# Performance work log

Hardware: AMD Instinct MI355X
Metric: run time of the kernel (lower is better)

Reference implementation:

```python
import jax, jax.numpy as jnp
import numpy as np

N_NODES = 100000
N_EDGES = 1600000
N_PAIRS = 200000
IN_CH = 128
HID_CH = 128


def _graph_conv(x, src, dst, edge_weight, w_rel, b_rel, w_root, num_nodes):
    # PyG GraphConv with aggr='mean':
    # out = lin_rel(mean_{j in N(i)}(x_j * w_ij)) + lin_root(x_i)
    msg = x[src] * edge_weight[:, None]                       # [E, C] gather
    agg = jax.ops.segment_sum(msg, dst, num_segments=num_nodes)  # [N, C]
    cnt = jax.ops.segment_sum(jnp.ones((src.shape[0],), x.dtype), dst,
                              num_segments=num_nodes)          # in-degree
    agg = agg / jnp.maximum(cnt, 1.0)[:, None]                 # mean aggr
    return agg @ w_rel + b_rel + x @ w_root


def setup_inputs() -> dict:
    key = jax.random.key(0)
    ks = jax.random.split(key, 10)
    x = jax.random.normal(ks[0], (N_NODES, IN_CH), dtype=jnp.float32)
    edge_index = jax.random.randint(ks[1], (2, N_EDGES), 0, N_NODES, dtype=jnp.int32)
    edge_weight = jax.random.uniform(ks[2], (N_EDGES,), dtype=jnp.float32)
    edge_label_index = jax.random.randint(ks[3], (2, N_PAIRS), 0, N_NODES, dtype=jnp.int32)
    s1 = 1.0 / np.sqrt(IN_CH)
    s2 = 1.0 / np.sqrt(HID_CH)
    w1_rel = jax.random.uniform(ks[4], (IN_CH, HID_CH), jnp.float32, -s1, s1)
    b1_rel = jnp.zeros((HID_CH,), jnp.float32)
    w1_root = jax.random.uniform(ks[5], (IN_CH, HID_CH), jnp.float32, -s1, s1)
    w2_rel = jax.random.uniform(ks[6], (HID_CH, HID_CH), jnp.float32, -s2, s2)
    b2_rel = jnp.zeros((HID_CH,), jnp.float32)
    w2_root = jax.random.uniform(ks[7], (HID_CH, HID_CH), jnp.float32, -s2, s2)
    return {"x": x, "edge_index": edge_index, "edge_weight": edge_weight,
            "edge_label_index": edge_label_index,
            "w1_rel": w1_rel, "b1_rel": b1_rel, "w1_root": w1_root,
            "w2_rel": w2_rel, "b2_rel": b2_rel, "w2_root": w2_root}


def reference(x, edge_index, edge_weight, edge_label_index,
              w1_rel, b1_rel, w1_root, w2_rel, b2_rel, w2_root):
    src, dst = edge_index[0], edge_index[1]
    # encode
    h = _graph_conv(x, src, dst, edge_weight, w1_rel, b1_rel, w1_root, x.shape[0])
    h = jax.nn.relu(h)
    z = _graph_conv(h, src, dst, edge_weight, w2_rel, b2_rel, w2_root, x.shape[0])
    # decode: scaled dot product between candidate pair embeddings
    zs = z[edge_label_index[0]]   # [P, H]
    zd = z[edge_label_index[1]]   # [P, H]
    scale = z.shape[-1] ** 0.5
    return jnp.sum(zs * zd, axis=-1) / scale
```

## Files before the change

### kernel.cpp

```cpp
#include <hip/hip_runtime.h>

#define NN 100000
#define NE 1600000
#define NP 200000
#define CH 128
#define LK 264

#define BSH 6
#define NB  1563
#define G1  256
#define EPB (NE / G1)
#define CAP3 4096
#define NCAST 6250

typedef _Float16 f16x8 __attribute__((ext_vector_type(8)));
typedef _Float16 f16x4 __attribute__((ext_vector_type(4)));
typedef float f32x4 __attribute__((ext_vector_type(4)));

__global__ __launch_bounds__(256)
void fused_prep_kernel(const float* __restrict__ x, _Float16* __restrict__ xh,
                       const int* __restrict__ dst, int* __restrict__ hist,
                       const float* __restrict__ w1r, const float* __restrict__ w1o,
                       const float* __restrict__ w2r, const float* __restrict__ w2o,
                       _Float16* __restrict__ w1t, _Float16* __restrict__ w2t) {
    __shared__ int s_h[NB];
    const int bb = blockIdx.x, tid = threadIdx.x;
    if (bb < NCAST) {
        int i = bb * 256 + tid;
        const float4* p = (const float4*)x + (size_t)i * 2;
        float4 a = p[0], b = p[1];
        f16x8 o = { (_Float16)a.x, (_Float16)a.y, (_Float16)a.z, (_Float16)a.w,
                    (_Float16)b.x, (_Float16)b.y, (_Float16)b.z, (_Float16)b.w };
        *((f16x8*)xh + i) = o;
    } else if (bb < NCAST + G1) {
        int g = bb - NCAST;
        for (int i = tid; i < NB; i += 256) s_h[i] = 0;
        __syncthreads();
        int start = g * EPB, end = start + EPB;
        for (int e = start + tid; e < end; e += 256)
            atomicAdd(&s_h[dst[e] >> BSH], 1);
        __syncthreads();
        int* row = hist + (size_t)g * NB;
        for (int i = tid; i < NB; i += 256) row[i] = s_h[i];
    } else {
        int idx = (bb - NCAST - G1) * 256 + tid;
        int which = idx >> 15;
        int li = idx & 32767;
        int n = li >> 8, k = li & 255;
        const float* wr = which ? w2r : w1r;
        const float* wo = which ? w2o : w1o;
        _Float16* wt = which ? w2t : w1t;
        float v = (k < 128) ? wr[k * 128 + n] : wo[(k - 128) * 128 + n];
        wt[li] = (_Float16)v;
    }
}

__global__ __launch_bounds__(256)
void colscan_kernel(int* __restrict__ hist, int* __restrict__ totals) {
    int b = blockIdx.x * 4 + (threadIdx.x >> 6);
    if (b >= NB) return;
    int lane = threadIdx.x & 63;
    size_t base = (size_t)(lane * 4) * NB + b;
    int v0 = hist[base];
    int v1 = hist[base + NB];
    int v2 = hist[base + 2 * (size_t)NB];
    int v3 = hist[base + 3 * (size_t)NB];
    int s0 = v0, s1 = s0 + v1, s2 = s1 + v2, s3 = s2 + v3;
    int incl = s3;
#pragma unroll
    for (int off = 1; off < 64; off <<= 1) {
        int n = __shfl_up(incl, off, 64);
        if (lane >= off) incl += n;
    }
    int excl = incl - s3;
    hist[base] = excl;
    hist[base + NB] = excl + s0;
    hist[base + 2 * (size_t)NB] = excl + s1;
    hist[base + 3 * (size_t)NB] = excl + s2;
    if (lane == 63) totals[b] = incl;
}

__global__ __launch_bounds__(1024)
void scanB_kernel(const int* __restrict__ totals, int* __restrict__ base) {
    __shared__ int s[2048];
    int tid = threadIdx.x;
    for (int i = tid; i < 2048; i += 1024) s[i] = (i < NB) ? totals[i] : 0;
    __syncthreads();
    for (int off = 1; off < 2048; off <<= 1) {
        int i0 = tid, i1 = tid + 1024;
        int v0 = (i0 >= off) ? s[i0 - off] : 0;
        int v1 = (i1 >= off) ? s[i1 - off] : 0;
        __syncthreads();
        s[i0] += v0; s[i1] += v1;
        __syncthreads();
    }
    if (tid == 0) base[0] = 0;
    for (int i = tid; i < NB; i += 1024) base[i + 1] = s[i];
}

__global__ __launch_bounds__(512)
void bucket_scatter_kernel(const int* __restrict__ src, const int* __restrict__ dst,
                           const float* __restrict__ ew, const int* __restrict__ hist,
                           const int* __restrict__ base, int2* __restrict__ tmp) {
    __shared__ int s_cur[NB];
    const int* row = hist + (size_t)blockIdx.x * NB;
    for (int i = threadIdx.x; i < NB; i += 512) s_cur[i] = base[i] + row[i];
    __syncthreads();
    int start = blockIdx.x * EPB, end = start + EPB;
    for (int e = start + threadIdx.x; e < end; e += 512) {
        int d = dst[e];
        int b = d >> BSH;
        int pos = atomicAdd(&s_cur[b], 1);
        tmp[pos] = make_int2(src[e] | ((d & 63) << 17), __float_as_int(ew[e]));
    }
}

__global__ __launch_bounds__(512)
void bucket_finalize_kernel(const int2* __restrict__ tmp, const int* __restrict__ base,
                            int* __restrict__ row_ptr, int2* __restrict__ csr, int N) {
    __shared__ int2 s_e[CAP3];
    __shared__ int s_cnt[64], s_off[64];
    int b = blockIdx.x;
    int lo = base[b], hi = base[b + 1];
    int size = hi - lo;
    int nbase = b << BSH;
    int ncnt = min(64, N - nbase);
    int tid = threadIdx.x;
    if (tid < 64) s_cnt[tid] = 0;
    bool inlds = (size <= CAP3);
    __syncthreads();
    if (inlds) {
        for (int i = tid; i < size; i += 512) {
            int2 e = tmp[lo + i];
            s_e[i] = e;
            atomicAdd(&s_cnt[(e.x >> 17) & 63], 1);
        }
    } else {
        for (int i = tid; i < size; i += 512) {
            int2 e = tmp[lo + i];
            atomicAdd(&s_cnt[(e.x >> 17) & 63], 1);
        }
    }
    __syncthreads();
    if (tid == 0) {
        int run = 0;
        for (int i = 0; i < 64; i++) { int v = s_cnt[i]; s_off[i] = run; s_cnt[i] = run; run += v; }
    }
    __syncthreads();
    if (tid < ncnt) row_ptr[nbase + tid] = lo + s_off[tid];
    if (b == NB - 1 && tid == 0) row_ptr[N] = hi;
    if (inlds) {
        for (int i = tid; i < size; i += 512) {
            int2 e = s_e[i];
            int dl = (e.x >> 17) & 63;
            int p = atomicAdd(&s_cnt[dl], 1);
            csr[lo + p] = make_int2(e.x & 0x1FFFF, e.y);
        }
    } else {
        for (int i = tid; i < size; i += 512) {
            int2 e = tmp[lo + i];
            int dl = (e.x >> 17) & 63;
            int p = atomicAdd(&s_cnt[dl], 1);
            csr[lo + p] = make_int2(e.x & 0x1FFFF, e.y);
        }
    }
}

template <bool RELU>
__global__ __launch_bounds__(512)
void gatherlayer_kernel(const _Float16* __restrict__ feat, const int* __restrict__ row_ptr,
                        const int2* __restrict__ csr, const _Float16* __restrict__ wt,
                        const float* __restrict__ bias, _Float16* __restrict__ out, int N) {
    __shared__ _Float16 atile[64][LK];

    const int tid = threadIdx.x;
    const int nb = blockIdx.x << BSH;
    const int wave = tid >> 6;
    const int lane = tid & 63;
    const int q = lane >> 4;
    const int l16 = lane & 15;
    const int c8 = l16 << 3;

    for (int nn = 0; nn < 8; nn++) {
        int local_n = wave * 8 + nn;
        int node = nb + local_n;
        if (node >= N) break;
        int r0 = row_ptr[node], r1 = row_ptr[node + 1];
        float acc[8] = {0.f, 0.f, 0.f, 0.f, 0.f, 0.f, 0.f, 0.f};
        int r = r0 + q;
        if (r < r1) {
            int2 e = csr[r];
            f16x8 v = *(const f16x8*)&feat[(size_t)e.x * CH + c8];
            int2 e2; f16x8 v2;
            bool h2 = (r + 4) < r1;
            if (h2) { e2 = csr[r + 4]; v2 = *(const f16x8*)&feat[(size_t)e2.x * CH + c8]; }
            for (int r3 = r + 8; r3 < r1; r3 += 4) {
                int2 e3 = csr[r3];
                f16x8 v3 = *(const f16x8*)&feat[(size_t)e3.x * CH + c8];
                float w = __int_as_float(e.y);
#pragma unroll
                for (int j = 0; j < 8; j++) acc[j] += w * (float)v[j];
                e = e2; v = v2;
                e2 = e3; v2 = v3;
            }
            float w = __int_as_float(e.y);
#pragma unroll
            for (int j = 0; j < 8; j++) acc[j] += w * (float)v[j];
            if (h2) {
                float w2 = __int_as_float(e2.y);
#pragma unroll
                for (int j = 0; j < 8; j++) acc[j] += w2 * (float)v2[j];
            }
        }
#pragma unroll
        for (int j = 0; j < 8; j++) {
            acc[j] += __shfl_xor(acc[j], 16, 64);
            acc[j] += __shfl_xor(acc[j], 32, 64);
        }
        if (q == 0) {
            float inv = 1.0f / fmaxf((float)(r1 - r0), 1.0f);
            f16x8 o;
#pragma unroll
            for (int j = 0; j < 8; j++) o[j] = (_Float16)(acc[j] * inv);
            *(f16x8*)&atile[local_n][c8] = o;
        }
    }

    for (int i = tid; i < 64 * 16; i += 512) {
        int rrow = i >> 4;
        int cc8 = (i & 15) << 3;
        int gn = nb + rrow;
        f16x8 v = {};
        if (gn < N) v = *(const f16x8*)&feat[(size_t)gn * CH + cc8];
        *(f16x8*)&atile[rrow][128 + cc8] = v;
    }
    __syncthreads();

    f32x4 ac[4];
#pragma unroll
    for (int m = 0; m < 4; m++) ac[m] = (f32x4){0.f, 0.f, 0.f, 0.f};

    const int ncol = wave * 16 + l16;
    const int kq = q * 8;
#pragma unroll
    for (int ks = 0; ks < 8; ks++) {
        int kbase = ks * 32 + kq;
        f16x8 bf = *(const f16x8*)&wt[(size_t)ncol * 256 + kbase];
#pragma unroll
        for (int m = 0; m < 4; m++) {
            f16x8 af = *(const f16x8*)&atile[m * 16 + l16][kbase];
            ac[m] = __builtin_amdgcn_mfma_f32_16x16x32_f16(af, bf, ac[m], 0, 0, 0);
        }
    }

    float bv = bias[ncol];
#pragma unroll
    for (int m = 0; m < 4; m++) {
#pragma unroll
        for (int r = 0; r < 4; r++) {
            int node = nb + m * 16 + q * 4 + r;
            if (node >= N) continue;
            float v = ac[m][r] + bv;
            if (RELU) v = fmaxf(v, 0.f);
            out[(size_t)node * CH + ncol] = (_Float16)v;
        }
    }
}

__global__ void decode_kernel(const _Float16* __restrict__ z,
                              const int* __restrict__ ps,
                              const int* __restrict__ pd,
                              float* __restrict__ out, int P) {
    long tid = (long)blockIdx.x * blockDim.x + threadIdx.x;
    int p = (int)(tid >> 5);
    int lane = (int)(tid & 31);
    if (p >= P) return;
    int s = ps[p], d = pd[p];
    f16x4 a = *(const f16x4*)&z[(size_t)s * CH + lane * 4];
    f16x4 b = *(const f16x4*)&z[(size_t)d * CH + lane * 4];
    float v = (float)a[0] * (float)b[0] + (float)a[1] * (float)b[1]
            + (float)a[2] * (float)b[2] + (float)a[3] * (float)b[3];
#pragma unroll
    for (int off = 16; off > 0; off >>= 1) v += __shfl_xor(v, off, 64);
    if (lane == 0) out[p] = v * 0.08838834764831845f;
}

extern "C" void kernel_launch(void* const* d_in, const int* in_sizes, int n_in,
                              void* d_out, int out_size, void* d_ws, size_t ws_size,
                              hipStream_t stream) {
    const float* x       = (const float*)d_in[0];
    const int*   ei      = (const int*)d_in[1];
    const float* ew      = (const float*)d_in[2];
    const int*   eli     = (const int*)d_in[3];
    const float* w1_rel  = (const float*)d_in[4];
    const float* b1      = (const float*)d_in[5];
    const float* w1_root = (const float*)d_in[6];
    const float* w2_rel  = (const float*)d_in[7];
    const float* b2      = (const float*)d_in[8];
    const float* w2_root = (const float*)d_in[9];
    float* out = (float*)d_out;

    const int N = NN, E = NE, P = NP;
    const size_t hrow = (size_t)N * CH * sizeof(_Float16);

    char* ws = (char*)d_ws;
    size_t off = 0;
    auto alloc = [&](size_t bytes) { char* p = ws + off; off = (off + bytes + 15) & ~(size_t)15; return p; };
    _Float16* xh  = (_Float16*)alloc(hrow);
    _Float16* hh  = (_Float16*)alloc(hrow);
    _Float16* zh  = (_Float16*)alloc(hrow);
    int* hist     = (int*)alloc((size_t)G1 * NB * 4);
    int* totals   = (int*)alloc((size_t)NB * 4);
    int* base     = (int*)alloc((size_t)(NB + 1) * 4);
    int* row_ptr  = (int*)alloc((size_t)(N + 1) * 4);
    int2* tmp     = (int2*)alloc((size_t)E * 8);
    int2* csr     = (int2*)alloc((size_t)E * 8);
    _Float16* w1t = (_Float16*)alloc((size_t)128 * 256 * 2);
    _Float16* w2t = (_Float16*)alloc((size_t)128 * 256 * 2);

    const int* src = ei;
    const int* dst = ei + E;

    fused_prep_kernel<<<NCAST + G1 + 256, 256, 0, stream>>>(
        x, xh, dst, hist, w1_rel, w1_root, w2_rel, w2_root, w1t, w2t);

    colscan_kernel<<<(NB + 3) / 4, 256, 0, stream>>>(hist, totals);
    scanB_kernel<<<1, 1024, 0, stream>>>(totals, base);
    bucket_scatter_kernel<<<G1, 512, 0, stream>>>(src, dst, ew, hist, base, tmp);
    bucket_finalize_kernel<<<NB, 512, 0, stream>>>(tmp, base, row_ptr, csr, N);

    gatherlayer_kernel<true><<<NB, 512, 0, stream>>>(xh, row_ptr, csr, w1t, b1, hh, N);
    gatherlayer_kernel<false><<<NB, 512, 0, stream>>>(hh, row_ptr, csr, w2t, b2, zh, N);

    {
        long threads = (long)P * 32;
        decode_kernel<<<(int)((threads + 255) / 256), 256, 0, stream>>>(zh, eli, eli + P, out, P);
    }
}
```

Before: 365.7 us.

## Replace two-level bucket sort CSR build with per-node global atomic counting sort

Replaces the bucketed histogram, column scan and two-pass bucket scatter/finalize with a direct per-node in-degree count using global atomics, a two-kernel scan into row_ptr, and a single scatter into CSR via global atomic cursors. This drops the intermediate tmp buffer, one full pass over the edges and several launches. In exchange it relies on global atomics over 100k counters instead of LDS atomics. Edge order within each row becomes nondeterministic, so floating-point summation order can vary between runs.

```diff
diff --git a/kernel.cpp b/kernel.cpp
--- a/kernel.cpp
+++ b/kernel.cpp
@@ -10,8 +10,8 @@
 #define NB  1563
 #define G1  256
 #define EPB (NE / G1)
-#define CAP3 4096
 #define NCAST 6250
+#define NSB 196
 
 typedef _Float16 f16x8 __attribute__((ext_vector_type(8)));
 typedef _Float16 f16x4 __attribute__((ext_vector_type(4)));
@@ -19,11 +19,10 @@
 
 __global__ __launch_bounds__(256)
 void fused_prep_kernel(const float* __restrict__ x, _Float16* __restrict__ xh,
-                       const int* __restrict__ dst, int* __restrict__ hist,
+                       const int* __restrict__ dst, int* __restrict__ cnt,
                        const float* __restrict__ w1r, const float* __restrict__ w1o,
                        const float* __restrict__ w2r, const float* __restrict__ w2o,
                        _Float16* __restrict__ w1t, _Float16* __restrict__ w2t) {
-    __shared__ int s_h[NB];
     const int bb = blockIdx.x, tid = threadIdx.x;
     if (bb < NCAST) {
         int i = bb * 256 + tid;
@@ -34,14 +33,9 @@
         *((f16x8*)xh + i) = o;
     } else if (bb < NCAST + G1) {
         int g = bb - NCAST;
-        for (int i = tid; i < NB; i += 256) s_h[i] = 0;
-        __syncthreads();
         int start = g * EPB, end = start + EPB;
         for (int e = start + tid; e < end; e += 256)
-            atomicAdd(&s_h[dst[e] >> BSH], 1);
-        __syncthreads();
-        int* row = hist + (size_t)g * NB;
-        for (int i = tid; i < NB; i += 256) row[i] = s_h[i];
+            atomicAdd(&cnt[dst[e]], 1);
     } else {
         int idx = (bb - NCAST - G1) * 256 + tid;
         int which = idx >> 15;
@@ -55,114 +49,81 @@
     }
 }
 
-__global__ __launch_bounds__(256)
-void colscan_kernel(int* __restrict__ hist, int* __restrict__ totals) {
-    int b = blockIdx.x * 4 + (threadIdx.x >> 6);
-    if (b >= NB) return;
-    int lane = threadIdx.x & 63;
-    size_t base = (size_t)(lane * 4) * NB + b;
-    int v0 = hist[base];
-    int v1 = hist[base + NB];
-    int v2 = hist[base + 2 * (size_t)NB];
-    int v3 = hist[base + 3 * (size_t)NB];
-    int s0 = v0, s1 = s0 + v1, s2 = s1 + v2, s3 = s2 + v3;
-    int incl = s3;
+__global__ __launch_bounds__(512)
+void nodecount_sum_kernel(const int* __restrict__ cnt, int* __restrict__ bsum) {
+    __shared__ int s_w[8];
+    const int b = blockIdx.x, tid = threadIdx.x;
+    const int lane = tid & 63, w = tid >> 6;
+    int i = b * 512 + tid;
+    int v = (i < NN) ? cnt[i] : 0;
+#pragma unroll
+    for (int off = 1; off < 64; off <<= 1) v += __shfl_xor(v, off, 64);
+    if (lane == 0) s_w[w] = v;
+    __syncthreads();
+    if (tid == 0) {
+        int t = 0;
+#pragma unroll
+        for (int j = 0; j < 8; j++) t += s_w[j];
+        bsum[b] = t;
+    }
+}
+
+__global__ __launch_bounds__(512)
+void rowptr_kernel(const int* __restrict__ cnt, const int* __restrict__ bsum,
+                   int* __restrict__ row_ptr, int* __restrict__ cur) {
+    __shared__ int s_w[8];
+    __shared__ int s_woff[8];
+    __shared__ int s_boff;
+    const int b = blockIdx.x, tid = threadIdx.x;
+    const int lane = tid & 63, w = tid >> 6;
+
+    int v = (tid < b) ? bsum[tid] : 0;
+#pragma unroll
+    for (int off = 1; off < 64; off <<= 1) v += __shfl_xor(v, off, 64);
+    if (lane == 0) s_w[w] = v;
+    __syncthreads();
+    if (tid == 0) {
+        int t = 0;
+#pragma unroll
+        for (int j = 0; j < 8; j++) t += s_w[j];
+        s_boff = t;
+    }
+    __syncthreads();
+
+    int i = b * 512 + tid;
+    int c = (i < NN) ? cnt[i] : 0;
+    int incl = c;
 #pragma unroll
     for (int off = 1; off < 64; off <<= 1) {
         int n = __shfl_up(incl, off, 64);
         if (lane >= off) incl += n;
     }
-    int excl = incl - s3;
-    hist[base] = excl;
-    hist[base + NB] = excl + s0;
-    hist[base + 2 * (size_t)NB] = excl + s1;
-    hist[base + 3 * (size_t)NB] = excl + s2;
-    if (lane == 63) totals[b] = incl;
-}
-
-__global__ __launch_bounds__(1024)
-void scanB_kernel(const int* __restrict__ totals, int* __restrict__ base) {
-    __shared__ int s[2048];
-    int tid = threadIdx.x;
-    for (int i = tid; i < 2048; i += 1024) s[i] = (i < NB) ? totals[i] : 0;
-    __syncthreads();
-    for (int off = 1; off < 2048; off <<= 1) {
-        int i0 = tid, i1 = tid + 1024;
-        int v0 = (i0 >= off) ? s[i0 - off] : 0;
-        int v1 = (i1 >= off) ? s[i1 - off] : 0;
-        __syncthreads();
-        s[i0] += v0; s[i1] += v1;
-        __syncthreads();
-    }
-    if (tid == 0) base[0] = 0;
-    for (int i = tid; i < NB; i += 1024) base[i + 1] = s[i];
+    if (lane == 63) s_w[w] = incl;
+    __syncthreads();
+    if (tid == 0) {
+        int run = 0;
+#pragma unroll
+        for (int j = 0; j < 8; j++) { int t = s_w[j]; s_woff[j] = run; run += t; }
+    }
+    __syncthreads();
+    int excl = s_boff + s_woff[w] + incl - c;
+    if (i < NN) {
+        row_ptr[i] = excl;
+        cur[i] = excl;
+    }
+    if (b == NSB - 1 && tid == 511) row_ptr[NN] = s_boff + s_woff[7] + incl;
 }
 
 __global__ __launch_bounds__(512)
-void bucket_scatter_kernel(const int* __restrict__ src, const int* __restrict__ dst,
-                           const float* __restrict__ ew, const int* __restrict__ hist,
-                           const int* __restrict__ base, int2* __restrict__ tmp) {
-    __shared__ int s_cur[NB];
-    const int* row = hist + (size_t)blockIdx.x * NB;
-    for (int i = threadIdx.x; i < NB; i += 512) s_cur[i] = base[i] + row[i];
-    __syncthreads();
+void edge_scatter_kernel(const int* __restrict__ src, const int* __restrict__ dst,
+                         const float* __restrict__ ew, int* __restrict__ cur,
+                         int2* __restrict__ csr) {
     int start = blockIdx.x * EPB, end = start + EPB;
+#pragma unroll 4
     for (int e = start + threadIdx.x; e < end; e += 512) {
         int d = dst[e];
-        int b = d >> BSH;
-        int pos = atomicAdd(&s_cur[b], 1);
-        tmp[pos] = make_int2(src[e] | ((d & 63) << 17), __float_as_int(ew[e]));
-    }
-}
-
-__global__ __launch_bounds__(512)
-void bucket_finalize_kernel(const int2* __restrict__ tmp, const int* __restrict__ base,
-                            int* __restrict__ row_ptr, int2* __restrict__ csr, int N) {
-    __shared__ int2 s_e[CAP3];
-    __shared__ int s_cnt[64], s_off[64];
-    int b = blockIdx.x;
-    int lo = base[b], hi = base[b + 1];
-    int size = hi - lo;
-    int nbase = b << BSH;
-    int ncnt = min(64, N - nbase);
-    int tid = threadIdx.x;
-    if (tid < 64) s_cnt[tid] = 0;
-    bool inlds = (size <= CAP3);
-    __syncthreads();
-    if (inlds) {
-        for (int i = tid; i < size; i += 512) {
-            int2 e = tmp[lo + i];
-            s_e[i] = e;
-            atomicAdd(&s_cnt[(e.x >> 17) & 63], 1);
-        }
-    } else {
-        for (int i = tid; i < size; i += 512) {
-            int2 e = tmp[lo + i];
-            atomicAdd(&s_cnt[(e.x >> 17) & 63], 1);
-        }
-    }
-    __syncthreads();
-    if (tid == 0) {
-        int run = 0;
-        for (int i = 0; i < 64; i++) { int v = s_cnt[i]; s_off[i] = run; s_cnt[i] = run; run += v; }
-    }
-    __syncthreads();
-    if (tid < ncnt) row_ptr[nbase + tid] = lo + s_off[tid];
-    if (b == NB - 1 && tid == 0) row_ptr[N] = hi;
-    if (inlds) {
-        for (int i = tid; i < size; i += 512) {
-            int2 e = s_e[i];
-            int dl = (e.x >> 17) & 63;
-            int p = atomicAdd(&s_cnt[dl], 1);
-            csr[lo + p] = make_int2(e.x & 0x1FFFF, e.y);
-        }
-    } else {
-        for (int i = tid; i < size; i += 512) {
-            int2 e = tmp[lo + i];
-            int dl = (e.x >> 17) & 63;
-            int p = atomicAdd(&s_cnt[dl], 1);
-            csr[lo + p] = make_int2(e.x & 0x1FFFF, e.y);
-        }
+        int pos = atomicAdd(&cur[d], 1);
+        csr[pos] = make_int2(src[e], __float_as_int(ew[e]));
     }
 }
 
@@ -309,11 +270,10 @@
     _Float16* xh  = (_Float16*)alloc(hrow);
     _Float16* hh  = (_Float16*)alloc(hrow);
     _Float16* zh  = (_Float16*)alloc(hrow);
-    int* hist     = (int*)alloc((size_t)G1 * NB * 4);
-    int* totals   = (int*)alloc((size_t)NB * 4);
-    int* base     = (int*)alloc((size_t)(NB + 1) * 4);
+    int* cnt      = (int*)alloc((size_t)N * 4);
+    int* bsum     = (int*)alloc((size_t)NSB * 4);
     int* row_ptr  = (int*)alloc((size_t)(N + 1) * 4);
-    int2* tmp     = (int2*)alloc((size_t)E * 8);
+    int* cur      = (int*)alloc((size_t)N * 4);
     int2* csr     = (int2*)alloc((size_t)E * 8);
     _Float16* w1t = (_Float16*)alloc((size_t)128 * 256 * 2);
     _Float16* w2t = (_Float16*)alloc((size_t)128 * 256 * 2);
@@ -321,13 +281,14 @@
     const int* src = ei;
     const int* dst = ei + E;
 
+    hipMemsetAsync(cnt, 0, (size_t)N * 4, stream);
+
     fused_prep_kernel<<<NCAST + G1 + 256, 256, 0, stream>>>(
-        x, xh, dst, hist, w1_rel, w1_root, w2_rel, w2_root, w1t, w2t);
-
-    colscan_kernel<<<(NB + 3) / 4, 256, 0, stream>>>(hist, totals);
-    scanB_kernel<<<1, 1024, 0, stream>>>(totals, base);
-    bucket_scatter_kernel<<<G1, 512, 0, stream>>>(src, dst, ew, hist, base, tmp);
-    bucket_finalize_kernel<<<NB, 512, 0, stream>>>(tmp, base, row_ptr, csr, N);
+        x, xh, dst, cnt, w1_rel, w1_root, w2_rel, w2_root, w1t, w2t);
+
+    nodecount_sum_kernel<<<NSB, 512, 0, stream>>>(cnt, bsum);
+    rowptr_kernel<<<NSB, 512, 0, stream>>>(cnt, bsum, row_ptr, cur);
+    edge_scatter_kernel<<<G1, 512, 0, stream>>>(src, dst, ew, cur, csr);
 
     gatherlayer_kernel<true><<<NB, 512, 0, stream>>>(xh, row_ptr, csr, w1t, b1, hh, N);
     gatherlayer_kernel<false><<<NB, 512, 0, stream>>>(hh, row_ptr, csr, w2t, b2, zh, N);
```

Result: slower. 504.8 us (+38.0%).

## Merge column scan and bucket-base scan via last-block counter; parallelize small scans

Applied to the files above, without the earlier changes.

Replaces the separate colscan and single-block scanB launches with one 25-block kernel. Each block scans 64 buckets across all 256 histogram rows, and the last block to finish, detected with an atomic counter plus thread fences, scans the bucket totals into base. It also swaps the serial 64-entry prefix in bucket_finalize for a wavefront shuffle scan. The decode kernel now has each half-wave load one full row as 16-byte vectors and exchange halves with shuffles. The intent is to cut one launch and its serialization, at the cost of a scan kernel with only 25 blocks whose threads walk 64 rows each with strided loads.

```diff
diff --git a/kernel.cpp b/kernel.cpp
--- a/kernel.cpp
+++ b/kernel.cpp
@@ -12,6 +12,7 @@
 #define EPB (NE / G1)
 #define CAP3 4096
 #define NCAST 6250
+#define CSG 25
 
 typedef _Float16 f16x8 __attribute__((ext_vector_type(8)));
 typedef _Float16 f16x4 __attribute__((ext_vector_type(4)));
@@ -22,7 +23,8 @@
                        const int* __restrict__ dst, int* __restrict__ hist,
                        const float* __restrict__ w1r, const float* __restrict__ w1o,
                        const float* __restrict__ w2r, const float* __restrict__ w2o,
-                       _Float16* __restrict__ w1t, _Float16* __restrict__ w2t) {
+                       _Float16* __restrict__ w1t, _Float16* __restrict__ w2t,
+                       int* __restrict__ sync) {
     __shared__ int s_h[NB];
     const int bb = blockIdx.x, tid = threadIdx.x;
     if (bb < NCAST) {
@@ -44,6 +46,7 @@
         for (int i = tid; i < NB; i += 256) row[i] = s_h[i];
     } else {
         int idx = (bb - NCAST - G1) * 256 + tid;
+        if (idx == 0) *sync = 0;
         int which = idx >> 15;
         int li = idx & 32767;
         int n = li >> 8, k = li & 255;
@@ -56,46 +59,82 @@
 }
 
 __global__ __launch_bounds__(256)
-void colscan_kernel(int* __restrict__ hist, int* __restrict__ totals) {
-    int b = blockIdx.x * 4 + (threadIdx.x >> 6);
-    if (b >= NB) return;
-    int lane = threadIdx.x & 63;
-    size_t base = (size_t)(lane * 4) * NB + b;
-    int v0 = hist[base];
-    int v1 = hist[base + NB];
-    int v2 = hist[base + 2 * (size_t)NB];
-    int v3 = hist[base + 3 * (size_t)NB];
-    int s0 = v0, s1 = s0 + v1, s2 = s1 + v2, s3 = s2 + v3;
-    int incl = s3;
+void colscan_kernel(int* __restrict__ hist, int* __restrict__ totals,
+                    int* __restrict__ base, int* __restrict__ sync) {
+    __shared__ int qs[4][64];
+    __shared__ int s_sync;
+    __shared__ int ws[4];
+    const int tid = threadIdx.x;
+    const int q = tid >> 6, lb = tid & 63;
+    const int b = blockIdx.x * 64 + lb;
+    const bool valid = (b < NB);
+
+    int s = 0;
+    if (valid) {
+        for (int g = q * 64; g < q * 64 + 64; ++g)
+            s += hist[(size_t)g * NB + b];
+    }
+    qs[q][lb] = s;
+    __syncthreads();
+
+    if (tid < 64) {
+        int a0 = qs[0][tid], a1 = qs[1][tid], a2 = qs[2][tid], a3 = qs[3][tid];
+        qs[0][tid] = 0;
+        qs[1][tid] = a0;
+        qs[2][tid] = a0 + a1;
+        qs[3][tid] = a0 + a1 + a2;
+        int bt = blockIdx.x * 64 + tid;
+        if (bt < NB) totals[bt] = a0 + a1 + a2 + a3;
+    }
+    __syncthreads();
+
+    int run = qs[q][lb];
+    if (valid) {
+        for (int g = q * 64; g < q * 64 + 64; ++g) {
+            size_t idx = (size_t)g * NB + b;
+            int v = hist[idx];
+            hist[idx] = run;
+            run += v;
+        }
+    }
+
+    __syncthreads();
+    if (tid == 0) {
+        __threadfence();
+        s_sync = atomicAdd(sync, 1);
+    }
+    __syncthreads();
+    if (s_sync != CSG - 1) return;
+    __threadfence();
+
+    const int c0 = tid * 7;
+    int incl7[7];
+    int cs = 0;
+#pragma unroll
+    for (int k = 0; k < 7; k++) {
+        int i = c0 + k;
+        int t = (i < NB) ? totals[i] : 0;
+        cs += t;
+        incl7[k] = cs;
+    }
+    int lane = tid & 63, w = tid >> 6;
+    int incl = cs;
 #pragma unroll
     for (int off = 1; off < 64; off <<= 1) {
         int n = __shfl_up(incl, off, 64);
         if (lane >= off) incl += n;
     }
-    int excl = incl - s3;
-    hist[base] = excl;
-    hist[base + NB] = excl + s0;
-    hist[base + 2 * (size_t)NB] = excl + s1;
-    hist[base + 3 * (size_t)NB] = excl + s2;
-    if (lane == 63) totals[b] = incl;
-}
-
-__global__ __launch_bounds__(1024)
-void scanB_kernel(const int* __restrict__ totals, int* __restrict__ base) {
-    __shared__ int s[2048];
-    int tid = threadIdx.x;
-    for (int i = tid; i < 2048; i += 1024) s[i] = (i < NB) ? totals[i] : 0;
-    __syncthreads();
-    for (int off = 1; off < 2048; off <<= 1) {
-        int i0 = tid, i1 = tid + 1024;
-        int v0 = (i0 >= off) ? s[i0 - off] : 0;
-        int v1 = (i1 >= off) ? s[i1 - off] : 0;
-        __syncthreads();
-        s[i0] += v0; s[i1] += v1;
-        __syncthreads();
-    }
+    if (lane == 63) ws[w] = incl;
+    __syncthreads();
+    int woff = 0;
+    for (int j = 0; j < w; j++) woff += ws[j];
+    int chunk_excl = woff + incl - cs;
     if (tid == 0) base[0] = 0;
-    for (int i = tid; i < NB; i += 1024) base[i + 1] = s[i];
+#pragma unroll
+    for (int k = 0; k < 7; k++) {
+        int i = c0 + k;
+        if (i < NB) base[i + 1] = chunk_excl + incl7[k];
+    }
 }
 
 __global__ __launch_bounds__(512)
@@ -142,9 +181,17 @@
         }
     }
     __syncthreads();
-    if (tid == 0) {
-        int run = 0;
-        for (int i = 0; i < 64; i++) { int v = s_cnt[i]; s_off[i] = run; s_cnt[i] = run; run += v; }
+    if (tid < 64) {
+        int v = s_cnt[tid];
+        int incl = v;
+#pragma unroll
+        for (int off = 1; off < 64; off <<= 1) {
+            int n = __shfl_up(incl, off, 64);
+            if (tid >= off) incl += n;
+        }
+        int excl = incl - v;
+        s_off[tid] = excl;
+        s_cnt[tid] = excl;
     }
     __syncthreads();
     if (tid < ncnt) row_ptr[nbase + tid] = lo + s_off[tid];
@@ -273,16 +320,25 @@
                               float* __restrict__ out, int P) {
     long tid = (long)blockIdx.x * blockDim.x + threadIdx.x;
     int p = (int)(tid >> 5);
-    int lane = (int)(tid & 31);
+    int lane32 = (int)(tid & 31);
     if (p >= P) return;
-    int s = ps[p], d = pd[p];
-    f16x4 a = *(const f16x4*)&z[(size_t)s * CH + lane * 4];
-    f16x4 b = *(const f16x4*)&z[(size_t)d * CH + lane * 4];
-    float v = (float)a[0] * (float)b[0] + (float)a[1] * (float)b[1]
-            + (float)a[2] * (float)b[2] + (float)a[3] * (float)b[3];
-#pragma unroll
-    for (int off = 16; off > 0; off >>= 1) v += __shfl_xor(v, off, 64);
-    if (lane == 0) out[p] = v * 0.08838834764831845f;
+    int l16 = lane32 & 15;
+    int half = lane32 >> 4;
+    int row = half ? pd[p] : ps[p];
+    int4 a = *(const int4*)&z[(size_t)row * CH + l16 * 8];
+    int4 b;
+    b.x = __shfl_xor(a.x, 16, 64);
+    b.y = __shfl_xor(a.y, 16, 64);
+    b.z = __shfl_xor(a.z, 16, 64);
+    b.w = __shfl_xor(a.w, 16, 64);
+    union U { int4 i; f16x8 h; };
+    U ua, ub; ua.i = a; ub.i = b;
+    float v = 0.f;
+#pragma unroll
+    for (int j = 0; j < 8; j++) v += (float)ua.h[j] * (float)ub.h[j];
+#pragma unroll
+    for (int off = 8; off > 0; off >>= 1) v += __shfl_xor(v, off, 64);
+    if (lane32 == 0) out[p] = v * 0.08838834764831845f;
 }
 
 extern "C" void kernel_launch(void* const* d_in, const int* in_sizes, int n_in,
@@ -313,6 +369,7 @@
     int* totals   = (int*)alloc((size_t)NB * 4);
     int* base     = (int*)alloc((size_t)(NB + 1) * 4);
     int* row_ptr  = (int*)alloc((size_t)(N + 1) * 4);
+    int* sync     = (int*)alloc(16);
     int2* tmp     = (int2*)alloc((size_t)E * 8);
     int2* csr     = (int2*)alloc((size_t)E * 8);
     _Float16* w1t = (_Float16*)alloc((size_t)128 * 256 * 2);
@@ -322,10 +379,9 @@
     const int* dst = ei + E;
 
     fused_prep_kernel<<<NCAST + G1 + 256, 256, 0, stream>>>(
-        x, xh, dst, hist, w1_rel, w1_root, w2_rel, w2_root, w1t, w2t);
-
-    colscan_kernel<<<(NB + 3) / 4, 256, 0, stream>>>(hist, totals);
-    scanB_kernel<<<1, 1024, 0, stream>>>(totals, base);
+        x, xh, dst, hist, w1_rel, w1_root, w2_rel, w2_root, w1t, w2t, sync);
+
+    colscan_kernel<<<CSG, 256, 0, stream>>>(hist, totals, base, sync);
     bucket_scatter_kernel<<<G1, 512, 0, stream>>>(src, dst, ew, hist, base, tmp);
     bucket_finalize_kernel<<<NB, 512, 0, stream>>>(tmp, base, row_ptr, csr, N);
 
```

After: 371.1 us. No clear change (+1.5%).
